# Performance work log

Measured on AMD Instinct MI355X. Metric: run time of the kernel, lower is better.

Reference implementation:

```python
import jax, jax.numpy as jnp
import numpy as np

D_MODEL = 1024
N_HEADS = 16
D_HEAD = D_MODEL // N_HEADS


def setup_inputs() -> dict:
    key = jax.random.key(0)
    k1, k2, k3 = jax.random.split(key, 3)
    x = jax.random.normal(k1, (2, 2048, D_MODEL), dtype=jnp.float32)
    # Dense layer params (glorot-ish scale)
    W_qkv = jax.random.normal(k2, (D_MODEL, 3 * D_MODEL), dtype=jnp.float32) * (1.0 / np.sqrt(D_MODEL))
    b_qkv = jnp.zeros((3 * D_MODEL,), dtype=jnp.float32)
    W_proj = jax.random.normal(k3, (D_MODEL, D_MODEL), dtype=jnp.float32) * (1.0 / np.sqrt(D_MODEL))
    b_proj = jnp.zeros((D_MODEL,), dtype=jnp.float32)
    return {"x": x, "W_qkv": W_qkv, "b_qkv": b_qkv, "W_proj": W_proj, "b_proj": b_proj}


def reference(x, W_qkv, b_qkv, W_proj, b_proj):
    B, S, _ = x.shape
    qkv = x @ W_qkv + b_qkv                      # [B,S,3D]
    q, k, v = jnp.split(qkv, 3, axis=-1)
    # [B,S,D] -> [B,H,S,Dh]
    def to_heads(t):
        return t.reshape(B, S, N_HEADS, D_HEAD).transpose(0, 2, 1, 3)
    q, k, v = to_heads(q), to_heads(k), to_heads(v)
    scores = jnp.einsum('bhqd,bhkd->bhqk', q, k)  # [B,H,S,S]
    causal = jnp.tril(jnp.ones((S, S), dtype=bool))
    # NOTE: mask applied BEFORE scaling, matching the original module.
    scores = jnp.where(causal[None, None, :, :], scores, jnp.float32(-1e9))
    scaled = scores / jnp.sqrt(jnp.float32(D_HEAD))
    attn = jax.nn.softmax(scaled, axis=-1)
    ctx = jnp.einsum('bhqk,bhkd->bhqd', attn, v)  # [B,H,S,Dh]
    ctx = ctx.transpose(0, 2, 1, 3).reshape(B, S, D_MODEL)
    return ctx @ W_proj + b_proj
```

## Files before the change

### kernel.cpp

```cpp
#include <hip/hip_runtime.h>
#include <stdint.h>

typedef __attribute__((ext_vector_type(8))) short short8;
typedef __attribute__((ext_vector_type(4))) float f32x4;

#define QSCALE 0.18033688011112043f

__device__ __forceinline__ unsigned short f2b(float f) {
  union { float f; uint32_t u; } v; v.f = f;
  uint32_t u = v.u;
  u = u + 0x7fffu + ((u >> 16) & 1u);
  return (unsigned short)(u >> 16);
}
__device__ __forceinline__ unsigned int cvtpk(float lo, float hi) {
  unsigned int r;
  asm("v_cvt_pk_bf16_f32 %0, %1, %2" : "=v"(r) : "v"(lo), "v"(hi));
  return r;
}
__device__ __forceinline__ void gload16(const void* g, void* lds) {
  __builtin_amdgcn_global_load_lds((const __attribute__((address_space(1))) void*)g,
                                   (__attribute__((address_space(3))) void*)lds, 16, 0, 0);
}

__global__ __launch_bounds__(256) void cvt_f32_bf16(const float* __restrict__ in,
                                                    unsigned short* __restrict__ out, int n) {
  int i = (blockIdx.x * 256 + threadIdx.x) * 4;
  if (i < n) {
    float4 v = *(const float4*)(in + i);
    ushort4 o;
    o.x = f2b(v.x); o.y = f2b(v.y); o.z = f2b(v.z); o.w = f2b(v.w);
    *(ushort4*)(out + i) = o;
  }
}

__global__ __launch_bounds__(256) void transposeW(const float* __restrict__ W,
                                                  unsigned short* __restrict__ Wt,
                                                  int K, int N, float scale, int scaleRows) {
  __shared__ float tile[32][33];
  int x0 = blockIdx.x * 32, y0 = blockIdx.y * 32;
  int tx = threadIdx.x, ty = threadIdx.y;
  #pragma unroll
  for (int j = 0; j < 4; ++j)
    tile[ty + j * 8][tx] = W[(size_t)(y0 + ty + j * 8) * N + x0 + tx];
  __syncthreads();
  #pragma unroll
  for (int j = 0; j < 4; ++j) {
    int orow = x0 + ty + j * 8;
    float s = (orow < scaleRows) ? scale : 1.0f;
    Wt[(size_t)orow * K + y0 + tx] = f2b(tile[tx][ty + j * 8] * s);
  }
}

template<bool OUTF32, int BN>
__global__ __launch_bounds__(256, 3) void gemm_bt(const unsigned short* __restrict__ A,
                                                  const unsigned short* __restrict__ Bt,
                                                  const float* __restrict__ bias,
                                                  void* __restrict__ outp,
                                                  unsigned short* __restrict__ vtOut,
                                                  int M, int N, int K,
                                                  float bscale, int bscaleN, int mtiles) {
  constexpr int FN = BN / 32;
  constexpr int BH = BN / 2;
  __shared__ unsigned short As[2][64 * 64];
  __shared__ unsigned short Bs[2][BH * 64];
  const int t = threadIdx.x;
  const int lane = t & 63;
  const int w = t >> 6;
  const int wm = w >> 1, wn = w & 1;

  const int cpx = gridDim.x >> 3;
  const int swz = (blockIdx.x & 7) * cpx + (blockIdx.x >> 3);
  const int m0 = (swz % mtiles) * 128;
  const int n0 = (swz / mtiles) * BN;

  const f32x4 zero = {0.f, 0.f, 0.f, 0.f};
  f32x4 acc[4][FN];
  #pragma unroll
  for (int i = 0; i < 4; ++i)
    #pragma unroll
    for (int j = 0; j < FN; ++j) acc[i][j] = zero;

  const int cl = lane & 15, g = lane >> 4;
  const int prow = t >> 3;
  const int pc   = (t & 7) ^ (prow & 7);

  auto stage = [&](int k0, int buf) {
    #pragma unroll
    for (int r = 0; r < 2; ++r) {
      int lrow = r * 32 + prow + 64 * (pc >> 2);
      gload16(A + (size_t)(m0 + lrow) * K + k0 + (pc & 3) * 8,
              (char*)As[buf] + r * 4096 + t * 16);
    }
    #pragma unroll
    for (int r = 0; r < BN / 64; ++r) {
      int lrow = r * 32 + prow + BH * (pc >> 2);
      gload16(Bt + (size_t)(n0 + lrow) * K + k0 + (pc & 3) * 8,
              (char*)Bs[buf] + r * 4096 + t * 16);
    }
  };

  stage(0, 0);
  __syncthreads();

  const int nk = K >> 5;
  for (int ki = 0; ki < nk; ++ki) {
    const int cur = ki & 1;
    if (ki + 1 < nk) stage((ki + 1) << 5, cur ^ 1);
    char* AsB = (char*)As[cur];
    char* BsB = (char*)Bs[cur];
    short8 af[4], bfr[FN];
    #pragma unroll
    for (int f = 0; f < 4; ++f) {
      int pr = f * 16 + cl;
      af[f] = *(const short8*)(AsB + pr * 128 + ((((wm << 2) + g) ^ (pr & 7)) << 4));
    }
    #pragma unroll
    for (int f = 0; f < FN; ++f) {
      int lr = wn * BH + f * 16 + cl;
      int pr = lr & (BH - 1);
      bfr[f] = *(const short8*)(BsB + pr * 128 + ((((wn << 2) + g) ^ (pr & 7)) << 4));
    }
    #pragma unroll
    for (int fm = 0; fm < 4; ++fm)
      #pragma unroll
      for (int fn = 0; fn < FN; ++fn)
        acc[fm][fn] = __builtin_amdgcn_mfma_f32_16x16x32_bf16(af[fm], bfr[fn], acc[fm][fn], 0, 0, 0);
    __syncthreads();
  }

  const bool vpath = (!OUTF32) && (vtOut != nullptr) && (n0 >= 2048);
  #pragma unroll
  for (int fn = 0; fn < FN; ++fn) {
    int col = n0 + wn * BH + fn * 16 + cl;
    float bv = bias[col] * ((col < bscaleN) ? bscale : 1.0f);
    if (vpath) {
      int hcol = col - 2048;
      size_t vrow = (size_t)hcol * 2048;
      #pragma unroll
      for (int fm = 0; fm < 4; ++fm) {
        int rbase = m0 + wm * 64 + fm * 16 + g * 4;
        int b = rbase >> 11, s = rbase & 2047;
        ushort4 ov;
        ov.x = f2b(acc[fm][fn][0] + bv);
        ov.y = f2b(acc[fm][fn][1] + bv);
        ov.z = f2b(acc[fm][fn][2] + bv);
        ov.w = f2b(acc[fm][fn][3] + bv);
        *(ushort4*)(vtOut + (size_t)b * 1024 * 2048 + vrow + s) = ov;
      }
    } else {
      #pragma unroll
      for (int fm = 0; fm < 4; ++fm) {
        int rbase = m0 + wm * 64 + fm * 16 + g * 4;
        #pragma unroll
        for (int r = 0; r < 4; ++r) {
          float vout = acc[fm][fn][r] + bv;
          if (OUTF32) ((float*)outp)[(size_t)(rbase + r) * N + col] = vout;
          else ((unsigned short*)outp)[(size_t)(rbase + r) * N + col] = f2b(vout);
        }
      }
    }
  }
}

__global__ __launch_bounds__(256, 3) void attn_mfma3(const unsigned short* __restrict__ qkv,
                                                     const unsigned short* __restrict__ Vt,
                                                     unsigned short* __restrict__ ctx) {
  const int idx = blockIdx.x;
  const int bh = ((idx & 7) << 2) | ((idx >> 3) & 3);
  const int qt = 31 - (idx >> 5);
  const int b = bh >> 4, h = bh & 15;
  const int t = threadIdx.x;
  const int l = t & 63;
  const int w = t >> 6;
  const int cl = l & 15;
  const int g  = l >> 4;

  __shared__ unsigned short Ks[2][64 * 64];
  __shared__ unsigned short Vs[2][64 * 64];
  __shared__ unsigned short Ps[4][16 * 64];
  __shared__ unsigned short Ones[16 * 64];

  char* Pbuf = (char*)(&Ps[w][0]);
  char* OnB = (char*)Ones;

  const size_t kbase  = (size_t)(b * 2048) * 3072 + 1024 + h * 64;
  const size_t vtbase = (size_t)(bh * 64) * 2048;

  auto stage = [&](int jt, int buf) {
    #pragma unroll
    for (int i = 0; i < 2; ++i) {
      int row = i * 32 + w * 8 + (l >> 3);
      int ch  = (l & 7) ^ (l >> 3);
      gload16(qkv + kbase + (size_t)(jt * 64 + row) * 3072 + ch * 8,
              (char*)Ks[buf] + i * 4096 + w * 1024);
      gload16(Vt + vtbase + (size_t)row * 2048 + jt * 64 + ch * 8,
              (char*)Vs[buf] + i * 4096 + w * 1024);
    }
  };

  {
    int row = t >> 4;
    int c4  = (t & 15) * 4;
    unsigned short vv = (row == 0) ? (unsigned short)0x3F80 : (unsigned short)0;
    ushort4 ov = {vv, vv, vv, vv};
    *(ushort4*)(OnB + ((row * 128 + c4 * 2) ^ ((row & 7) << 4))) = ov;
  }

  stage(0, 0);
  __syncthreads();

  short8 a5[2];
  #pragma unroll
  for (int kk = 0; kk < 2; ++kk)
    a5[kk] = *(const short8*)(OnB + ((cl * 128 + kk * 64 + g * 16) ^ ((cl & 7) << 4)));

  short8 bq[2];
  {
    const unsigned short* qp = qkv + (size_t)(b * 2048 + qt * 64 + w * 16 + cl) * 3072 + h * 64 + g * 8;
    bq[0] = *(const short8*)(qp);
    bq[1] = *(const short8*)(qp + 32);
  }

  f32x4 o[4], o5;
  #pragma unroll
  for (int c = 0; c < 4; ++c) o[c] = (f32x4){0.f, 0.f, 0.f, 0.f};
  o5 = (f32x4){0.f, 0.f, 0.f, 0.f};
  float m = -1e30f;

  for (int jt = 0; jt <= qt; ++jt) {
    const int cur = jt & 1;
    if (jt < qt) stage(jt + 1, cur ^ 1);
    char* KsB = (char*)Ks[cur];
    char* VsB = (char*)Vs[cur];

    short8 ak[4][2];
    #pragma unroll
    for (int tt = 0; tt < 4; ++tt)
      #pragma unroll
      for (int kk = 0; kk < 2; ++kk)
        ak[tt][kk] = *(const short8*)(KsB + (((tt * 16 + cl) * 128 + kk * 64 + g * 16) ^ ((cl & 7) << 4)));
    short8 av[4][2];
    #pragma unroll
    for (int c = 0; c < 4; ++c)
      #pragma unroll
      for (int kk = 0; kk < 2; ++kk)
        av[c][kk] = *(const short8*)(VsB + (((c * 16 + cl) * 128 + kk * 64 + g * 16) ^ ((cl & 7) << 4)));

    f32x4 st[4];
    #pragma unroll
    for (int tt = 0; tt < 4; ++tt) st[tt] = (f32x4){0.f, 0.f, 0.f, 0.f};
    __builtin_amdgcn_s_setprio(1);
    #pragma unroll
    for (int kk = 0; kk < 2; ++kk)
      #pragma unroll
      for (int tt = 0; tt < 4; ++tt)
        st[tt] = __builtin_amdgcn_mfma_f32_16x16x32_bf16(ak[tt][kk], bq[kk], st[tt], 0, 0, 0);
    __builtin_amdgcn_s_setprio(0);

    float z[4][4];
    #pragma unroll
    for (int tt = 0; tt < 4; ++tt)
      #pragma unroll
      for (int r = 0; r < 4; ++r) z[tt][r] = st[tt][r];
    if (jt == qt) {
      int q_loc = w * 16 + cl;
      #pragma unroll
      for (int tt = 0; tt < 4; ++tt)
        #pragma unroll
        for (int r = 0; r < 4; ++r)
          if (tt * 16 + 4 * g + r > q_loc) z[tt][r] = -1e30f;
    }
    float m0a = fmaxf(fmaxf(z[0][0], z[0][1]), fmaxf(z[0][2], z[0][3]));
    float m1a = fmaxf(fmaxf(z[1][0], z[1][1]), fmaxf(z[1][2], z[1][3]));
    float m2a = fmaxf(fmaxf(z[2][0], z[2][1]), fmaxf(z[2][2], z[2][3]));
    float m3a = fmaxf(fmaxf(z[3][0], z[3][1]), fmaxf(z[3][2], z[3][3]));
    float cm = fmaxf(fmaxf(m0a, m1a), fmaxf(m2a, m3a));
    cm = fmaxf(cm, __shfl_xor(cm, 16));
    cm = fmaxf(cm, __shfl_xor(cm, 32));

    if (!__all(cm <= m + 8.f)) {
      float mn = fmaxf(m, cm);
      float alpha = exp2f(m - mn);
      m = mn;
      #pragma unroll
      for (int c = 0; c < 4; ++c)
        #pragma unroll
        for (int r = 0; r < 4; ++r) o[c][r] *= alpha;
      o5[0] *= alpha;
    }

    #pragma unroll
    for (int tt = 0; tt < 4; ++tt) {
      float p0 = exp2f(z[tt][0] - m), p1 = exp2f(z[tt][1] - m);
      float p2 = exp2f(z[tt][2] - m), p3 = exp2f(z[tt][3] - m);
      uint2 val;
      val.x = cvtpk(p0, p1);
      val.y = cvtpk(p2, p3);
      *(uint2*)(Pbuf + ((cl * 128 + tt * 32 + g * 8) ^ ((cl & 7) << 4))) = val;
    }
    short8 bp[2];
    #pragma unroll
    for (int kk = 0; kk < 2; ++kk)
      bp[kk] = *(const short8*)(Pbuf + ((cl * 128 + kk * 64 + g * 16) ^ ((cl & 7) << 4)));

    __builtin_amdgcn_s_setprio(1);
    #pragma unroll
    for (int kk = 0; kk < 2; ++kk) {
      #pragma unroll
      for (int c = 0; c < 4; ++c)
        o[c] = __builtin_amdgcn_mfma_f32_16x16x32_bf16(av[c][kk], bp[kk], o[c], 0, 0, 0);
      o5 = __builtin_amdgcn_mfma_f32_16x16x32_bf16(a5[kk], bp[kk], o5, 0, 0, 0);
    }
    __builtin_amdgcn_s_setprio(0);

    __syncthreads();
  }

  float lsum = __shfl(o5[0], cl);
  float inv = 1.f / lsum;
  unsigned short* crow = ctx + (size_t)(b * 2048 + qt * 64 + w * 16 + cl) * 1024 + h * 64 + g * 4;
  #pragma unroll
  for (int c = 0; c < 4; ++c) {
    uint2 val;
    val.x = cvtpk(o[c][0] * inv, o[c][1] * inv);
    val.y = cvtpk(o[c][2] * inv, o[c][3] * inv);
    *(uint2*)(crow + c * 16) = val;
  }
}

extern "C" void kernel_launch(void* const* d_in, const int* in_sizes, int n_in,
                              void* d_out, int out_size, void* d_ws, size_t ws_size,
                              hipStream_t stream) {
  const float* x     = (const float*)d_in[0];
  const float* Wqkv  = (const float*)d_in[1];
  const float* bqkv  = (const float*)d_in[2];
  const float* Wproj = (const float*)d_in[3];
  const float* bproj = (const float*)d_in[4];
  float* out = (float*)d_out;

  char* ws = (char*)d_ws;
  unsigned short* xb     = (unsigned short*)(ws);
  unsigned short* wqkvT  = (unsigned short*)(ws + 8388608);
  unsigned short* wprojT = (unsigned short*)(ws + 14680064);
  unsigned short* qkv    = (unsigned short*)(ws + 16777216);
  unsigned short* ctx    = (unsigned short*)(ws + 41943040);
  unsigned short* vt     = (unsigned short*)(ws + 50331648);

  cvt_f32_bf16<<<4096, 256, 0, stream>>>(x, xb, 4096 * 1024);

  dim3 tb(32, 8);
  transposeW<<<dim3(3072 / 32, 1024 / 32), tb, 0, stream>>>(Wqkv, wqkvT, 1024, 3072, QSCALE, 1024);
  transposeW<<<dim3(1024 / 32, 1024 / 32), tb, 0, stream>>>(Wproj, wprojT, 1024, 1024, 1.0f, 0);

  gemm_bt<false, 128><<<768, 256, 0, stream>>>(xb, wqkvT, bqkv, qkv, vt,
                                               4096, 3072, 1024, QSCALE, 1024, 32);

  attn_mfma3<<<1024, 256, 0, stream>>>(qkv, vt, ctx);

  gemm_bt<true, 64><<<512, 256, 0, stream>>>(ctx, wprojT, bproj, out, nullptr,
                                             4096, 1024, 1024, 1.0f, 0, 32);
}
```

Baseline: 181.5 us.

## Merge prep kernels into one launch, drop LDS ones tile, raise attention occupancy

Combines the x conversion and both weight transposes into one kernel launch with block-index dispatch, removing two launches. In the attention kernel, the all-ones row-sum operand is now built directly in registers instead of LDS, and the Ones LDS buffer is removed. Occupancy hint rises from 3 to 4 blocks per CU. Freeing LDS and registers may allow more waves per CU, but the tighter launch bound can cause spills.

```diff
diff --git a/kernel.cpp b/kernel.cpp
--- a/kernel.cpp
+++ b/kernel.cpp
@@ -22,23 +22,30 @@
                                    (__attribute__((address_space(3))) void*)lds, 16, 0, 0);
 }
 
-__global__ __launch_bounds__(256) void cvt_f32_bf16(const float* __restrict__ in,
-                                                    unsigned short* __restrict__ out, int n) {
-  int i = (blockIdx.x * 256 + threadIdx.x) * 4;
-  if (i < n) {
-    float4 v = *(const float4*)(in + i);
+__global__ __launch_bounds__(256) void prep(const float* __restrict__ x,
+                                            unsigned short* __restrict__ xb,
+                                            const float* __restrict__ Wq,
+                                            unsigned short* __restrict__ WqT,
+                                            const float* __restrict__ Wp,
+                                            unsigned short* __restrict__ WpT) {
+  const int id = blockIdx.x;
+  const int t = threadIdx.x;
+  if (id < 4096) {
+    int i = id * 1024 + t * 4;
+    float4 v = *(const float4*)(x + i);
     ushort4 o;
     o.x = f2b(v.x); o.y = f2b(v.y); o.z = f2b(v.z); o.w = f2b(v.w);
-    *(ushort4*)(out + i) = o;
-  }
-}
-
-__global__ __launch_bounds__(256) void transposeW(const float* __restrict__ W,
-                                                  unsigned short* __restrict__ Wt,
-                                                  int K, int N, float scale, int scaleRows) {
+    *(ushort4*)(xb + i) = o;
+    return;
+  }
   __shared__ float tile[32][33];
-  int x0 = blockIdx.x * 32, y0 = blockIdx.y * 32;
-  int tx = threadIdx.x, ty = threadIdx.y;
+  const float* W; unsigned short* Wt; int N; float scale; int scaleRows; int bi;
+  if (id < 7168) { W = Wq; Wt = WqT; N = 3072; scale = QSCALE; scaleRows = 1024; bi = id - 4096; }
+  else           { W = Wp; Wt = WpT; N = 1024; scale = 1.0f;   scaleRows = 0;    bi = id - 7168; }
+  const int K = 1024;
+  const int nbx = N / 32;
+  const int x0 = (bi % nbx) * 32, y0 = (bi / nbx) * 32;
+  const int tx = t & 31, ty = t >> 5;
   #pragma unroll
   for (int j = 0; j < 4; ++j)
     tile[ty + j * 8][tx] = W[(size_t)(y0 + ty + j * 8) * N + x0 + tx];
@@ -162,7 +169,7 @@
   }
 }
 
-__global__ __launch_bounds__(256, 3) void attn_mfma3(const unsigned short* __restrict__ qkv,
+__global__ __launch_bounds__(256, 4) void attn_mfma3(const unsigned short* __restrict__ qkv,
                                                      const unsigned short* __restrict__ Vt,
                                                      unsigned short* __restrict__ ctx) {
   const int idx = blockIdx.x;
@@ -178,10 +185,8 @@
   __shared__ unsigned short Ks[2][64 * 64];
   __shared__ unsigned short Vs[2][64 * 64];
   __shared__ unsigned short Ps[4][16 * 64];
-  __shared__ unsigned short Ones[16 * 64];
 
   char* Pbuf = (char*)(&Ps[w][0]);
-  char* OnB = (char*)Ones;
 
   const size_t kbase  = (size_t)(b * 2048) * 3072 + 1024 + h * 64;
   const size_t vtbase = (size_t)(bh * 64) * 2048;
@@ -198,21 +203,15 @@
     }
   };
 
-  {
-    int row = t >> 4;
-    int c4  = (t & 15) * 4;
-    unsigned short vv = (row == 0) ? (unsigned short)0x3F80 : (unsigned short)0;
-    ushort4 ov = {vv, vv, vv, vv};
-    *(ushort4*)(OnB + ((row * 128 + c4 * 2) ^ ((row & 7) << 4))) = ov;
-  }
-
   stage(0, 0);
   __syncthreads();
 
-  short8 a5[2];
-  #pragma unroll
-  for (int kk = 0; kk < 2; ++kk)
-    a5[kk] = *(const short8*)(OnB + ((cl * 128 + kk * 64 + g * 16) ^ ((cl & 7) << 4)));
+  short8 a5;
+  {
+    short hv = (cl == 0) ? (short)0x3F80 : (short)0;
+    #pragma unroll
+    for (int j = 0; j < 8; ++j) a5[j] = hv;
+  }
 
   short8 bq[2];
   {
@@ -309,7 +308,7 @@
       #pragma unroll
       for (int c = 0; c < 4; ++c)
         o[c] = __builtin_amdgcn_mfma_f32_16x16x32_bf16(av[c][kk], bp[kk], o[c], 0, 0, 0);
-      o5 = __builtin_amdgcn_mfma_f32_16x16x32_bf16(a5[kk], bp[kk], o5, 0, 0, 0);
+      o5 = __builtin_amdgcn_mfma_f32_16x16x32_bf16(a5, bp[kk], o5, 0, 0, 0);
     }
     __builtin_amdgcn_s_setprio(0);
 
@@ -346,11 +345,7 @@
   unsigned short* ctx    = (unsigned short*)(ws + 41943040);
   unsigned short* vt     = (unsigned short*)(ws + 50331648);
 
-  cvt_f32_bf16<<<4096, 256, 0, stream>>>(x, xb, 4096 * 1024);
-
-  dim3 tb(32, 8);
-  transposeW<<<dim3(3072 / 32, 1024 / 32), tb, 0, stream>>>(Wqkv, wqkvT, 1024, 3072, QSCALE, 1024);
-  transposeW<<<dim3(1024 / 32, 1024 / 32), tb, 0, stream>>>(Wproj, wprojT, 1024, 1024, 1.0f, 0);
+  prep<<<8192, 256, 0, stream>>>(x, xb, Wqkv, wqkvT, Wproj, wprojT);
 
   gemm_bt<false, 128><<<768, 256, 0, stream>>>(xb, wqkvT, bqkv, qkv, vt,
                                                4096, 3072, 1024, QSCALE, 1024, 32);
```

Result: slower. 186.5 us (+2.8%).
